# Performance work log

Measured on AMD Instinct MI355X. Metric: run time of the kernel, lower is better.

Reference implementation:

```python
import jax, jax.numpy as jnp
import numpy as np

B = 16384          # batch size (positions)
NNZ_PER = 32       # active features per position (pieces on board)
F = 768            # 2 colors x 6 pieces x 64 squares
H = 512            # hidden_size


def setup_inputs() -> dict:
    key = jax.random.key(0)
    k1, k2, k3, k4, k5, k6 = jax.random.split(key, 6)
    nnz = B * NNZ_PER
    batch_row = jnp.repeat(jnp.arange(B, dtype=jnp.int64), NNZ_PER)
    stm_feat = jax.random.randint(k1, (nnz,), 0, F, dtype=jnp.int64)
    nstm_feat = jax.random.randint(k2, (nnz,), 0, F, dtype=jnp.int64)
    stm_indices = jnp.stack([batch_row, stm_feat])    # [2, nnz] COO (batch, feature)
    nstm_indices = jnp.stack([batch_row, nstm_feat])  # [2, nnz]
    stm_values = jnp.ones((nnz,), dtype=jnp.float32)   # binary features
    nstm_values = jnp.ones((nnz,), dtype=jnp.float32)
    W_ft = jax.random.normal(k3, (H, F), dtype=jnp.float32) * 0.02
    b_ft = jax.random.normal(k4, (H,), dtype=jnp.float32) * 0.02
    W_out = jax.random.normal(k5, (1, 2 * H), dtype=jnp.float32) * 0.02
    b_out = jax.random.normal(k6, (1,), dtype=jnp.float32) * 0.02
    return {
        "stm_indices": stm_indices,
        "nstm_indices": nstm_indices,
        "stm_values": stm_values,
        "nstm_values": nstm_values,
        "batch_size": B,
        "W_ft": W_ft,
        "b_ft": b_ft,
        "W_out": W_out,
        "b_out": b_out,
    }


def _to_dense(indices, values, batch_size):
    # torch.sparse_coo_tensor(...).to_dense(): duplicates are summed.
    dense = jnp.zeros((batch_size, F), dtype=jnp.float32)
    return dense.at[indices[0], indices[1]].add(values)


def reference(stm_indices, nstm_indices, stm_values, nstm_values, batch_size,
              W_ft, b_ft, W_out, b_out):
    stm_dense = _to_dense(stm_indices, stm_values, batch_size)     # [B, 768]
    nstm_dense = _to_dense(nstm_indices, nstm_values, batch_size)  # [B, 768]
    stm_hidden = stm_dense @ W_ft.T + b_ft     # [B, H]
    nstm_hidden = nstm_dense @ W_ft.T + b_ft   # [B, H]
    hidden = jnp.concatenate([stm_hidden, nstm_hidden], axis=1)  # [B, 2H]
    hidden = jnp.clip(hidden, 0.0, 1.0)
    return jax.nn.sigmoid(hidden @ W_out.T + b_out)  # [B, 1]
```

## Files before the change

kernel.cpp:

```cpp
#include <hip/hip_runtime.h>
#include <hip/hip_fp16.h>

#define B_SZ    16384
#define NNZ_PER 32
#define F_DIM   768
#define H_DIM   512

typedef unsigned int  uint32;
typedef unsigned long long uint64;
typedef unsigned char uchar;

__device__ inline uchar f32_to_e5m2(float x) {
    __half h = __float2half_rn(x);
    unsigned short hb = *(unsigned short*)&h;
    unsigned short lsb = (hb >> 8) & 1;
    hb = (unsigned short)(hb + 0x7F + lsb);
    return (uchar)(hb >> 8);
}

__global__ __launch_bounds__(256) void transpose_convert(
    const float* __restrict__ W, uchar* __restrict__ Wt8)
{
    __shared__ float tile[32][33];
    const int f0 = blockIdx.x * 32;
    const int h0 = blockIdx.y * 32;
    const int tx = threadIdx.x;
    const int ty = threadIdx.y;

#pragma unroll
    for (int i = 0; i < 32; i += 8)
        tile[ty + i][tx] = W[(h0 + ty + i) * F_DIM + f0 + tx];
    __syncthreads();
#pragma unroll
    for (int i = 0; i < 32; i += 8)
        Wt8[(size_t)(f0 + ty + i) * H_DIM + h0 + tx] = f32_to_e5m2(tile[tx][ty + i]);
}

__global__ __launch_bounds__(256, 4) void nnue_fwd(
    const int*   __restrict__ stm_idx,
    const int*   __restrict__ nstm_idx,
    const float* __restrict__ stm_val,
    const float* __restrict__ nstm_val,
    const uchar* __restrict__ Wt8,
    const float* __restrict__ b_ft,
    const float* __restrict__ W_out,
    const float* __restrict__ b_out,
    float* __restrict__ out)
{
    const int tid  = threadIdx.x;
    const int w    = tid >> 6;
    const int lane = tid & 63;
    const int half = lane >> 5;
    const int c    = lane & 31;
    const int b    = blockIdx.x * 4 + w;
    const int NNZ  = B_SZ * NNZ_PER;

    __shared__ uint64 sh[4][64];
    {
        const int base = b * NNZ_PER;
        int f; float v;
        if (lane < 32) { f = stm_idx [NNZ + base + lane];        v = stm_val [base + lane]; }
        else           { f = nstm_idx[NNZ + base + (lane - 32)]; v = nstm_val[base + (lane - 32)]; }
        __half2 vv = __float2half2_rn(v);
        sh[w][lane] = ((uint64)(*(uint32*)&vv) << 32) | (uint32)f;
    }
    __syncthreads();

    const uint32 selA = 0x01040004u;
    const uint32 selB = 0x03040204u;
    const uint32 coff = (uint32)c << 4;
    const char*  Wb   = (const char*)Wt8;

    __half2 z = __float2half2_rn(0.f);
    __half2 sa[8] = {z,z,z,z,z,z,z,z};
    __half2 na[8] = {z,z,z,z,z,z,z,z};

    uint4   bufA[8], bufB[8];
    __half2 valA[8], valB[8];

#define LOAD_GROUP(g, BUF, VAL)                                               \
    {                                                                         \
        _Pragma("unroll")                                                     \
        for (int i = 0; i < 8; ++i) {                                         \
            const int j = 4 * (g) + (i & 3);                                  \
            const int slot = (i < 4 ? 0 : 32) + 2 * j + half;                 \
            uint64 e  = sh[w][slot];                                          \
            uint32 f  = (uint32)e;                                            \
            uint32 v2 = (uint32)(e >> 32);                                    \
            VAL[i] = *(__half2*)&v2;                                          \
            BUF[i] = *(const uint4*)(Wb + (((size_t)f) << 9) + coff);         \
        }                                                                     \
    }

#define FMA_GROUP(BUF, VAL)                                                   \
    {                                                                         \
        _Pragma("unroll")                                                     \
        for (int i = 0; i < 8; ++i) {                                         \
            __half2* acc = (i < 4) ? sa : na;                                 \
            uint4 wv = BUF[i];                                                \
            __half2 vv = VAL[i];                                              \
            uint32 p;                                                         \
            p = __builtin_amdgcn_perm(0u, wv.x, selA); acc[0] = __hfma2(*(__half2*)&p, vv, acc[0]); \
            p = __builtin_amdgcn_perm(0u, wv.x, selB); acc[1] = __hfma2(*(__half2*)&p, vv, acc[1]); \
            p = __builtin_amdgcn_perm(0u, wv.y, selA); acc[2] = __hfma2(*(__half2*)&p, vv, acc[2]); \
            p = __builtin_amdgcn_perm(0u, wv.y, selB); acc[3] = __hfma2(*(__half2*)&p, vv, acc[3]); \
            p = __builtin_amdgcn_perm(0u, wv.z, selA); acc[4] = __hfma2(*(__half2*)&p, vv, acc[4]); \
            p = __builtin_amdgcn_perm(0u, wv.z, selB); acc[5] = __hfma2(*(__half2*)&p, vv, acc[5]); \
            p = __builtin_amdgcn_perm(0u, wv.w, selA); acc[6] = __hfma2(*(__half2*)&p, vv, acc[6]); \
            p = __builtin_amdgcn_perm(0u, wv.w, selB); acc[7] = __hfma2(*(__half2*)&p, vv, acc[7]); \
        }                                                                     \
    }

    LOAD_GROUP(0, bufA, valA);
    LOAD_GROUP(1, bufB, valB);
    FMA_GROUP(bufA, valA);
    LOAD_GROUP(2, bufA, valA);
    FMA_GROUP(bufB, valB);
    LOAD_GROUP(3, bufB, valB);
    FMA_GROUP(bufA, valA);
    FMA_GROUP(bufB, valB);

#undef LOAD_GROUP
#undef FMA_GROUP

    float s[16], n[16];
#pragma unroll
    for (int k = 0; k < 8; ++k) {
        int mi = *(int*)&sa[k];
        int oi = __shfl_xor(mi, 32, 64);
        __half2 o = *(__half2*)&oi;
        s[2 * k]     = __low2float(sa[k])  + __low2float(o);
        s[2 * k + 1] = __high2float(sa[k]) + __high2float(o);
        mi = *(int*)&na[k];
        oi = __shfl_xor(mi, 32, 64);
        o  = *(__half2*)&oi;
        n[2 * k]     = __low2float(na[k])  + __low2float(o);
        n[2 * k + 1] = __high2float(na[k]) + __high2float(o);
    }

    const float* bias = b_ft + c * 16;
    const float* wo   = W_out + half * H_DIM + c * 16;
    float dot = 0.f;
#pragma unroll
    for (int k = 0; k < 16; ++k) {
        float hv = half ? n[k] : s[k];
        float a  = fminf(fmaxf(hv + bias[k], 0.f), 1.f);
        dot += a * wo[k];
    }

#pragma unroll
    for (int off = 32; off > 0; off >>= 1)
        dot += __shfl_xor(dot, off, 64);

    if (lane == 0)
        out[b] = 1.f / (1.f + expf(-(dot + b_out[0])));
}

extern "C" void kernel_launch(void* const* d_in, const int* in_sizes, int n_in,
                              void* d_out, int out_size, void* d_ws, size_t ws_size,
                              hipStream_t stream) {
    const int*   stm_idx  = (const int*)  d_in[0];
    const int*   nstm_idx = (const int*)  d_in[1];
    const float* stm_val  = (const float*)d_in[2];
    const float* nstm_val = (const float*)d_in[3];
    const float* W_ft     = (const float*)d_in[5];
    const float* b_ft     = (const float*)d_in[6];
    const float* W_out    = (const float*)d_in[7];
    const float* b_out    = (const float*)d_in[8];
    float*       out      = (float*)d_out;
    uchar*       Wt8      = (uchar*)d_ws;

    dim3 tb(32, 8);
    dim3 tg(F_DIM / 32, H_DIM / 32);
    transpose_convert<<<tg, tb, 0, stream>>>(W_ft, Wt8);

    nnue_fwd<<<B_SZ / 4, 256, 0, stream>>>(stm_idx, nstm_idx, stm_val, nstm_val,
                                           Wt8, b_ft, W_out, b_out, out);
}
```

Measured before the change: 102.4 us.

## Split each position's hidden dimension across two waves with 8-byte loads

Each position is now handled by two wavefronts, each covering half of the hidden units. Every lane loads 8 bytes of e5m2 weights per feature instead of 16, and the per-position partial dot products are combined through shared memory after a second barrier. This halves the per-thread register footprint and doubles the number of waves, and launch bounds are raised to allow more resident blocks for latency hiding. In exchange it doubles the index/shared-memory setup per weight byte, adds a block-level sync, and issues smaller memory transactions.

```diff
diff --git a/kernel.cpp b/kernel.cpp
--- a/kernel.cpp
+++ b/kernel.cpp
@@ -36,7 +36,7 @@
         Wt8[(size_t)(f0 + ty + i) * H_DIM + h0 + tx] = f32_to_e5m2(tile[tx][ty + i]);
 }
 
-__global__ __launch_bounds__(256, 4) void nnue_fwd(
+__global__ __launch_bounds__(256, 6) void nnue_fwd(
     const int*   __restrict__ stm_idx,
     const int*   __restrict__ nstm_idx,
     const float* __restrict__ stm_val,
@@ -49,33 +49,39 @@
 {
     const int tid  = threadIdx.x;
     const int w    = tid >> 6;
+    const int pos  = w >> 1;
+    const int hh   = w & 1;
     const int lane = tid & 63;
     const int half = lane >> 5;
     const int c    = lane & 31;
-    const int b    = blockIdx.x * 4 + w;
+    const int b    = blockIdx.x * 2 + pos;
     const int NNZ  = B_SZ * NNZ_PER;
 
-    __shared__ uint64 sh[4][64];
-    {
-        const int base = b * NNZ_PER;
+    __shared__ uint64 sh[2][64];
+    __shared__ float  pdot[2][2];
+
+    if (tid < 128) {
+        const int p    = tid >> 6;
+        const int s    = tid & 63;
+        const int base = (blockIdx.x * 2 + p) * NNZ_PER;
         int f; float v;
-        if (lane < 32) { f = stm_idx [NNZ + base + lane];        v = stm_val [base + lane]; }
-        else           { f = nstm_idx[NNZ + base + (lane - 32)]; v = nstm_val[base + (lane - 32)]; }
+        if (s < 32) { f = stm_idx [NNZ + base + s];        v = stm_val [base + s]; }
+        else        { f = nstm_idx[NNZ + base + (s - 32)]; v = nstm_val[base + (s - 32)]; }
         __half2 vv = __float2half2_rn(v);
-        sh[w][lane] = ((uint64)(*(uint32*)&vv) << 32) | (uint32)f;
+        sh[p][s] = ((uint64)(*(uint32*)&vv) << 32) | (uint32)f;
     }
     __syncthreads();
 
     const uint32 selA = 0x01040004u;
     const uint32 selB = 0x03040204u;
-    const uint32 coff = (uint32)c << 4;
+    const uint32 coff = ((uint32)hh << 8) | ((uint32)c << 3);
     const char*  Wb   = (const char*)Wt8;
 
     __half2 z = __float2half2_rn(0.f);
-    __half2 sa[8] = {z,z,z,z,z,z,z,z};
-    __half2 na[8] = {z,z,z,z,z,z,z,z};
+    __half2 sa[4] = {z, z, z, z};
+    __half2 na[4] = {z, z, z, z};
 
-    uint4   bufA[8], bufB[8];
+    uint2   bufA[8], bufB[8];
     __half2 valA[8], valB[8];
 
 #define LOAD_GROUP(g, BUF, VAL)                                               \
@@ -84,11 +90,12 @@
         for (int i = 0; i < 8; ++i) {                                         \
             const int j = 4 * (g) + (i & 3);                                  \
             const int slot = (i < 4 ? 0 : 32) + 2 * j + half;                 \
-            uint64 e  = sh[w][slot];                                          \
+            uint64 e  = sh[pos][slot];                                        \
             uint32 f  = (uint32)e;                                            \
             uint32 v2 = (uint32)(e >> 32);                                    \
             VAL[i] = *(__half2*)&v2;                                          \
-            BUF[i] = *(const uint4*)(Wb + (((size_t)f) << 9) + coff);         \
+            uint32 off = (f << 9) | coff;                                     \
+            BUF[i] = *(const uint2*)(Wb + off);                               \
         }                                                                     \
     }
 
@@ -97,17 +104,13 @@
         _Pragma("unroll")                                                     \
         for (int i = 0; i < 8; ++i) {                                         \
             __half2* acc = (i < 4) ? sa : na;                                 \
-            uint4 wv = BUF[i];                                                \
+            uint2 wv = BUF[i];                                                \
             __half2 vv = VAL[i];                                              \
             uint32 p;                                                         \
             p = __builtin_amdgcn_perm(0u, wv.x, selA); acc[0] = __hfma2(*(__half2*)&p, vv, acc[0]); \
             p = __builtin_amdgcn_perm(0u, wv.x, selB); acc[1] = __hfma2(*(__half2*)&p, vv, acc[1]); \
             p = __builtin_amdgcn_perm(0u, wv.y, selA); acc[2] = __hfma2(*(__half2*)&p, vv, acc[2]); \
             p = __builtin_amdgcn_perm(0u, wv.y, selB); acc[3] = __hfma2(*(__half2*)&p, vv, acc[3]); \
-            p = __builtin_amdgcn_perm(0u, wv.z, selA); acc[4] = __hfma2(*(__half2*)&p, vv, acc[4]); \
-            p = __builtin_amdgcn_perm(0u, wv.z, selB); acc[5] = __hfma2(*(__half2*)&p, vv, acc[5]); \
-            p = __builtin_amdgcn_perm(0u, wv.w, selA); acc[6] = __hfma2(*(__half2*)&p, vv, acc[6]); \
-            p = __builtin_amdgcn_perm(0u, wv.w, selB); acc[7] = __hfma2(*(__half2*)&p, vv, acc[7]); \
         }                                                                     \
     }
 
@@ -123,29 +126,24 @@
 #undef LOAD_GROUP
 #undef FMA_GROUP
 
-    float s[16], n[16];
-#pragma unroll
-    for (int k = 0; k < 8; ++k) {
-        int mi = *(int*)&sa[k];
-        int oi = __shfl_xor(mi, 32, 64);
-        __half2 o = *(__half2*)&oi;
-        s[2 * k]     = __low2float(sa[k])  + __low2float(o);
-        s[2 * k + 1] = __high2float(sa[k]) + __high2float(o);
-        mi = *(int*)&na[k];
-        oi = __shfl_xor(mi, 32, 64);
-        o  = *(__half2*)&oi;
-        n[2 * k]     = __low2float(na[k])  + __low2float(o);
-        n[2 * k + 1] = __high2float(na[k]) + __high2float(o);
-    }
-
-    const float* bias = b_ft + c * 16;
-    const float* wo   = W_out + half * H_DIM + c * 16;
+    const float* bias = b_ft  + (hh << 8) + (c << 3);
+    const float* wo   = W_out + half * H_DIM + (hh << 8) + (c << 3);
     float dot = 0.f;
 #pragma unroll
-    for (int k = 0; k < 16; ++k) {
-        float hv = half ? n[k] : s[k];
-        float a  = fminf(fmaxf(hv + bias[k], 0.f), 1.f);
-        dot += a * wo[k];
+    for (int k = 0; k < 4; ++k) {
+        int ms = *(int*)&sa[k];
+        int mn = *(int*)&na[k];
+        int os = __shfl_xor(ms, 32, 64);
+        int on = __shfl_xor(mn, 32, 64);
+        int mm = half ? mn : ms;
+        int oo = half ? on : os;
+        __half2 mh = *(__half2*)&mm;
+        __half2 oh = *(__half2*)&oo;
+        float h0 = __low2float(mh)  + __low2float(oh);
+        float h1 = __high2float(mh) + __high2float(oh);
+        float a0 = fminf(fmaxf(h0 + bias[2 * k],     0.f), 1.f);
+        float a1 = fminf(fmaxf(h1 + bias[2 * k + 1], 0.f), 1.f);
+        dot += a0 * wo[2 * k] + a1 * wo[2 * k + 1];
     }
 
 #pragma unroll
@@ -153,7 +151,13 @@
         dot += __shfl_xor(dot, off, 64);
 
     if (lane == 0)
-        out[b] = 1.f / (1.f + expf(-(dot + b_out[0])));
+        pdot[pos][hh] = dot;
+    __syncthreads();
+
+    if (hh == 0 && lane == 0) {
+        float d = pdot[pos][0] + pdot[pos][1] + b_out[0];
+        out[b] = 1.f / (1.f + expf(-d));
+    }
 }
 
 extern "C" void kernel_launch(void* const* d_in, const int* in_sizes, int n_in,
@@ -174,6 +178,6 @@
     dim3 tg(F_DIM / 32, H_DIM / 32);
     transpose_convert<<<tg, tb, 0, stream>>>(W_ft, Wt8);
 
-    nnue_fwd<<<B_SZ / 4, 256, 0, stream>>>(stm_idx, nstm_idx, stm_val, nstm_val,
+    nnue_fwd<<<B_SZ / 2, 256, 0, stream>>>(stm_idx, nstm_idx, stm_val, nstm_val,
                                            Wt8, b_ft, W_out, b_out, out);
 }
```

Result: slower. 109.4 us (+6.8%).

## Remap wave lanes to hidden units with scalar feature indices

Applied to the files above, without the earlier changes.

Each lane now owns 8 hidden units across all 32 features, instead of two half-waves splitting the features with 16 units each. Feature indices are loaded as wave-uniform scalars via readfirstlane, and only values go through shared memory. This removes the cross-half shuffle reduction and the per-lane LDS index reads. It uses narrower 8-byte weight loads, pipelines 8 groups, and raises the occupancy hint from 4 to 6. The trade-off is twice as many load instructions per feature and higher scalar register pressure from 64 scalar indices.

```diff
diff --git a/kernel.cpp b/kernel.cpp
--- a/kernel.cpp
+++ b/kernel.cpp
@@ -36,7 +36,7 @@
         Wt8[(size_t)(f0 + ty + i) * H_DIM + h0 + tx] = f32_to_e5m2(tile[tx][ty + i]);
 }
 
-__global__ __launch_bounds__(256, 4) void nnue_fwd(
+__global__ __launch_bounds__(256, 6) void nnue_fwd(
     const int*   __restrict__ stm_idx,
     const int*   __restrict__ nstm_idx,
     const float* __restrict__ stm_val,
@@ -50,102 +50,97 @@
     const int tid  = threadIdx.x;
     const int w    = tid >> 6;
     const int lane = tid & 63;
-    const int half = lane >> 5;
-    const int c    = lane & 31;
     const int b    = blockIdx.x * 4 + w;
     const int NNZ  = B_SZ * NNZ_PER;
+    const int ub   = __builtin_amdgcn_readfirstlane(b) * NNZ_PER;
 
-    __shared__ uint64 sh[4][64];
+    __shared__ uint32 sv[4][64];
     {
-        const int base = b * NNZ_PER;
-        int f; float v;
-        if (lane < 32) { f = stm_idx [NNZ + base + lane];        v = stm_val [base + lane]; }
-        else           { f = nstm_idx[NNZ + base + (lane - 32)]; v = nstm_val[base + (lane - 32)]; }
+        const int k    = lane & 31;
+        const int side = lane >> 5;
+        float v = (lane < 32) ? stm_val[ub + k] : nstm_val[ub + k];
         __half2 vv = __float2half2_rn(v);
-        sh[w][lane] = ((uint64)(*(uint32*)&vv) << 32) | (uint32)f;
+        sv[w][side * 32 + (k & 1) * 16 + (k >> 1)] = *(uint32*)&vv;
     }
     __syncthreads();
 
+    int sf[32], nf[32];
+#pragma unroll
+    for (int k = 0; k < 32; ++k) {
+        sf[k] = __builtin_amdgcn_readfirstlane(stm_idx [NNZ + ub + k]);
+        nf[k] = __builtin_amdgcn_readfirstlane(nstm_idx[NNZ + ub + k]);
+    }
+
     const uint32 selA = 0x01040004u;
     const uint32 selB = 0x03040204u;
-    const uint32 coff = (uint32)c << 4;
     const char*  Wb   = (const char*)Wt8;
+    const uint32 loff = (uint32)(lane << 3);
 
     __half2 z = __float2half2_rn(0.f);
-    __half2 sa[8] = {z,z,z,z,z,z,z,z};
-    __half2 na[8] = {z,z,z,z,z,z,z,z};
+    __half2 se[4] = {z,z,z,z}, so[4] = {z,z,z,z};
+    __half2 ne[4] = {z,z,z,z}, no[4] = {z,z,z,z};
 
-    uint4   bufA[8], bufB[8];
-    __half2 valA[8], valB[8];
+    uint2 bufA[8], bufB[8];
 
-#define LOAD_GROUP(g, BUF, VAL)                                               \
+#define LOAD_GROUP(g, BUF)                                                    \
     {                                                                         \
+        const int* IDX = ((g) >= 4) ? nf : sf;                                \
+        const int  gg  = (g) & 3;                                             \
         _Pragma("unroll")                                                     \
-        for (int i = 0; i < 8; ++i) {                                         \
-            const int j = 4 * (g) + (i & 3);                                  \
-            const int slot = (i < 4 ? 0 : 32) + 2 * j + half;                 \
-            uint64 e  = sh[w][slot];                                          \
-            uint32 f  = (uint32)e;                                            \
-            uint32 v2 = (uint32)(e >> 32);                                    \
-            VAL[i] = *(__half2*)&v2;                                          \
-            BUF[i] = *(const uint4*)(Wb + (((size_t)f) << 9) + coff);         \
+        for (int i = 0; i < 4; ++i) {                                         \
+            BUF[i]     = *(const uint2*)(Wb + (((size_t)IDX[8*gg + 2*i    ]) << 9) + loff); \
+            BUF[4 + i] = *(const uint2*)(Wb + (((size_t)IDX[8*gg + 2*i + 1]) << 9) + loff); \
         }                                                                     \
     }
 
-#define FMA_GROUP(BUF, VAL)                                                   \
+#define FMA_GROUP(g, BUF, ACCE, ACCO)                                         \
     {                                                                         \
+        const uint32* vb = &sv[w][((g) >= 4) ? 32 : 0];                       \
+        uint4 ve = *(const uint4*)(vb + 4 * ((g) & 3));                       \
+        uint4 vo = *(const uint4*)(vb + 16 + 4 * ((g) & 3));                  \
+        uint32 va[8] = {ve.x, ve.y, ve.z, ve.w, vo.x, vo.y, vo.z, vo.w};      \
         _Pragma("unroll")                                                     \
         for (int i = 0; i < 8; ++i) {                                         \
-            __half2* acc = (i < 4) ? sa : na;                                 \
-            uint4 wv = BUF[i];                                                \
-            __half2 vv = VAL[i];                                              \
+            __half2* A = (i < 4) ? ACCE : ACCO;                               \
+            __half2 vv = *(__half2*)&va[i];                                   \
+            uint2 wv = BUF[i];                                                \
             uint32 p;                                                         \
-            p = __builtin_amdgcn_perm(0u, wv.x, selA); acc[0] = __hfma2(*(__half2*)&p, vv, acc[0]); \
-            p = __builtin_amdgcn_perm(0u, wv.x, selB); acc[1] = __hfma2(*(__half2*)&p, vv, acc[1]); \
-            p = __builtin_amdgcn_perm(0u, wv.y, selA); acc[2] = __hfma2(*(__half2*)&p, vv, acc[2]); \
-            p = __builtin_amdgcn_perm(0u, wv.y, selB); acc[3] = __hfma2(*(__half2*)&p, vv, acc[3]); \
-            p = __builtin_amdgcn_perm(0u, wv.z, selA); acc[4] = __hfma2(*(__half2*)&p, vv, acc[4]); \
-            p = __builtin_amdgcn_perm(0u, wv.z, selB); acc[5] = __hfma2(*(__half2*)&p, vv, acc[5]); \
-            p = __builtin_amdgcn_perm(0u, wv.w, selA); acc[6] = __hfma2(*(__half2*)&p, vv, acc[6]); \
-            p = __builtin_amdgcn_perm(0u, wv.w, selB); acc[7] = __hfma2(*(__half2*)&p, vv, acc[7]); \
+            p = __builtin_amdgcn_perm(0u, wv.x, selA); A[0] = __hfma2(*(__half2*)&p, vv, A[0]); \
+            p = __builtin_amdgcn_perm(0u, wv.x, selB); A[1] = __hfma2(*(__half2*)&p, vv, A[1]); \
+            p = __builtin_amdgcn_perm(0u, wv.y, selA); A[2] = __hfma2(*(__half2*)&p, vv, A[2]); \
+            p = __builtin_amdgcn_perm(0u, wv.y, selB); A[3] = __hfma2(*(__half2*)&p, vv, A[3]); \
         }                                                                     \
     }
 
-    LOAD_GROUP(0, bufA, valA);
-    LOAD_GROUP(1, bufB, valB);
-    FMA_GROUP(bufA, valA);
-    LOAD_GROUP(2, bufA, valA);
-    FMA_GROUP(bufB, valB);
-    LOAD_GROUP(3, bufB, valB);
-    FMA_GROUP(bufA, valA);
-    FMA_GROUP(bufB, valB);
+    LOAD_GROUP(0, bufA);
+    LOAD_GROUP(1, bufB);
+    FMA_GROUP(0, bufA, se, so);  LOAD_GROUP(2, bufA);
+    FMA_GROUP(1, bufB, se, so);  LOAD_GROUP(3, bufB);
+    FMA_GROUP(2, bufA, se, so);  LOAD_GROUP(4, bufA);
+    FMA_GROUP(3, bufB, se, so);  LOAD_GROUP(5, bufB);
+    FMA_GROUP(4, bufA, ne, no);  LOAD_GROUP(6, bufA);
+    FMA_GROUP(5, bufB, ne, no);  LOAD_GROUP(7, bufB);
+    FMA_GROUP(6, bufA, ne, no);
+    FMA_GROUP(7, bufB, ne, no);
 
 #undef LOAD_GROUP
 #undef FMA_GROUP
 
-    float s[16], n[16];
-#pragma unroll
-    for (int k = 0; k < 8; ++k) {
-        int mi = *(int*)&sa[k];
-        int oi = __shfl_xor(mi, 32, 64);
-        __half2 o = *(__half2*)&oi;
-        s[2 * k]     = __low2float(sa[k])  + __low2float(o);
-        s[2 * k + 1] = __high2float(sa[k]) + __high2float(o);
-        mi = *(int*)&na[k];
-        oi = __shfl_xor(mi, 32, 64);
-        o  = *(__half2*)&oi;
-        n[2 * k]     = __low2float(na[k])  + __low2float(o);
-        n[2 * k + 1] = __high2float(na[k]) + __high2float(o);
-    }
-
-    const float* bias = b_ft + c * 16;
-    const float* wo   = W_out + half * H_DIM + c * 16;
+    const int hbase = lane << 3;
     float dot = 0.f;
 #pragma unroll
-    for (int k = 0; k < 16; ++k) {
-        float hv = half ? n[k] : s[k];
-        float a  = fminf(fmaxf(hv + bias[k], 0.f), 1.f);
-        dot += a * wo[k];
+    for (int q = 0; q < 4; ++q) {
+        float s0 = __low2float(se[q])  + __low2float(so[q]);
+        float s1 = __high2float(se[q]) + __high2float(so[q]);
+        float n0 = __low2float(ne[q])  + __low2float(no[q]);
+        float n1 = __high2float(ne[q]) + __high2float(no[q]);
+        float b0 = b_ft[hbase + 2*q];
+        float b1 = b_ft[hbase + 2*q + 1];
+        float a;
+        a = fminf(fmaxf(s0 + b0, 0.f), 1.f); dot += a * W_out[hbase + 2*q];
+        a = fminf(fmaxf(s1 + b1, 0.f), 1.f); dot += a * W_out[hbase + 2*q + 1];
+        a = fminf(fmaxf(n0 + b0, 0.f), 1.f); dot += a * W_out[H_DIM + hbase + 2*q];
+        a = fminf(fmaxf(n1 + b1, 0.f), 1.f); dot += a * W_out[H_DIM + hbase + 2*q + 1];
     }
 
 #pragma unroll
```

Result: slower. 108.2 us (+5.7%).
